# Optimization experiments

Measured on AMD Instinct MI355X. Metric: run time of the kernel, lower is better.

## Reference

```python
import jax, jax.numpy as jnp
import numpy as np

B, L, D_OUT, D_HIDDEN = 16, 4096, 1024, 512
MAX_PHASE = 6.28
R_MIN, R_MAX = 0.9, 0.999


def setup_inputs() -> dict:
    key = jax.random.key(0)
    ks = jax.random.split(key, 8)
    x = jax.random.normal(ks[0], (B, L, D_OUT), dtype=jnp.float32)
    # theta_init: log(max_phase * u)
    u_th = jax.random.uniform(ks[1], (D_HIDDEN,), dtype=jnp.float32)
    theta_log = jnp.log(MAX_PHASE * u_th)
    # nu_init: log(-0.5 * log(u * (r_max^2 - r_min^2) + r_min^2))
    u_nu = jax.random.uniform(ks[2], (D_HIDDEN,), dtype=jnp.float32)
    nu_log = jnp.log(-0.5 * jnp.log(u_nu * (R_MAX**2 - R_MIN**2) + R_MIN**2))
    # gamma_log_init from (nu_log, theta_log)
    diag_lambda = jnp.exp(-jnp.exp(nu_log) + 1j * jnp.exp(theta_log))
    gamma_log = jnp.log(jnp.sqrt(1.0 - jnp.abs(diag_lambda) ** 2))
    b_norm = jnp.sqrt(2.0 * D_OUT)
    c_norm = jnp.sqrt(float(D_HIDDEN))
    B_re = jax.random.normal(ks[3], (D_HIDDEN, D_OUT), dtype=jnp.float32) / b_norm
    B_im = jax.random.normal(ks[4], (D_HIDDEN, D_OUT), dtype=jnp.float32) / b_norm
    C_re = jax.random.normal(ks[5], (D_OUT, D_HIDDEN), dtype=jnp.float32) / c_norm
    C_im = jax.random.normal(ks[6], (D_OUT, D_HIDDEN), dtype=jnp.float32) / c_norm
    D = jax.random.normal(ks[7], (D_OUT,), dtype=jnp.float32)
    return {"x": x, "theta_log": theta_log, "nu_log": nu_log, "gamma_log": gamma_log,
            "B_re": B_re, "B_im": B_im, "C_re": C_re, "C_im": C_im, "D": D}


def _binop(q_i, q_j):
    # associative op for linear recurrence h_t = A_t * h_{t-1} + b_t (diagonal A)
    A_i, b_i = q_i
    A_j, b_j = q_j
    return (A_j * A_i, A_j * b_i + b_j)


def reference(x, theta_log, nu_log, gamma_log, B_re, B_im, C_re, C_im, D):
    diag_lambda = jnp.exp(-jnp.exp(nu_log) + 1j * jnp.exp(theta_log))  # (H,)
    B_norm = (B_re + 1j * B_im) * jnp.exp(gamma_log)[:, None]          # (H, D)
    C = C_re + 1j * C_im                                               # (D, H)
    # input projection: Bu_t = B_norm @ x_t -> (B, L, H) complex
    Bu = jnp.einsum('hd,bld->blh', B_norm, x.astype(B_norm.dtype))
    Lam = jnp.broadcast_to(diag_lambda, Bu.shape)
    # parallel scan over the sequence axis
    _, h = jax.lax.associative_scan(_binop, (Lam, Bu), axis=1)         # (B, L, H)
    # readout: y_t = Re[C h_t] + D * x_t
    y = jnp.einsum('oh,blh->blo', C, h).real + D * x
    return (y, h[:, -1])
```

## Files before the change

kernel.cpp:

```cpp
#include <hip/hip_runtime.h>

#define NB 16
#define NL 4096
#define NDO 1024
#define NH 512
#define NM (NB*NL)
#define NK 1024
#define NN 1024
#define CH 128
#define NCHUNK (NL/CH)
#define YCOUNT ((size_t)NM*NDO)
#define HCOUNT ((size_t)NB*NH)

typedef unsigned short u16;
typedef float f32x4 __attribute__((ext_vector_type(4)));
typedef unsigned int u32x4 __attribute__((ext_vector_type(4)));
typedef __bf16 bf16x8 __attribute__((ext_vector_type(8)));

__device__ __forceinline__ u16 f2bf(float f){
  unsigned u = __float_as_uint(f);
  unsigned r = u + 0x7fffu + ((u >> 16) & 1u);
  return (u16)(r >> 16);
}
__device__ __forceinline__ float bf2f(u16 v){ return __uint_as_float(((unsigned)v) << 16); }
__device__ __forceinline__ unsigned pack2(float a, float b){
  return (unsigned)f2bf(a) | ((unsigned)f2bf(b) << 16);
}

__device__ __forceinline__ void gld_lds16(const u16* g, u16* l){
  __builtin_amdgcn_global_load_lds(
      (const __attribute__((address_space(1))) unsigned int*)g,
      (__attribute__((address_space(3))) unsigned int*)l,
      16, 0, 0);
}


__global__ void prep_w1(const float* __restrict__ Bre, const float* __restrict__ Bim,
                        const float* __restrict__ gl, u16* __restrict__ W1){
  int i = blockIdx.x * blockDim.x + threadIdx.x;
  if (i >= NH * NDO) return;
  int h = i / NDO, d = i % NDO;
  float g = expf(gl[h]);
  W1[(size_t)h * NK + d]        = f2bf(Bre[i] * g);
  W1[(size_t)(NH + h) * NK + d] = f2bf(Bim[i] * g);
}

__global__ void prep_w2(const float* __restrict__ Cre, const float* __restrict__ Cim,
                        u16* __restrict__ W2){
  int i = blockIdx.x * blockDim.x + threadIdx.x;
  if (i >= NDO * NH) return;
  int o = i / NH, k = i % NH;
  W2[(size_t)o * NK + k]      = f2bf(Cre[i]);
  W2[(size_t)o * NK + NH + k] = f2bf(-Cim[i]);
}

__global__ void prep_lam(const float* __restrict__ theta_log, const float* __restrict__ nu_log,
                         float* __restrict__ lam){
  int h = threadIdx.x;
  if (h >= NH) return;
  float nu = expf(nu_log[h]);
  float th = expf(theta_log[h]);
  float mag = expf(-nu);
  float lre = mag * cosf(th), lim = mag * sinf(th);
  double pre = (double)lre, pim = (double)lim;
  #pragma unroll
  for (int s = 0; s < 7; s++){
    double nr = pre*pre - pim*pim;
    double ni = 2.0*pre*pim;
    pre = nr; pim = ni;
  }
  lam[h]        = lre;
  lam[NH + h]   = lim;
  lam[2*NH + h] = (float)pre;
  lam[3*NH + h] = (float)pim;
}

__global__ __launch_bounds__(256) void convert_x(const float* __restrict__ X, u16* __restrict__ Xb){
  size_t i = ((size_t)blockIdx.x * 256 + threadIdx.x) * 8;
  f32x4 a = *(const f32x4*)(X + i);
  f32x4 b = *(const f32x4*)(X + i + 4);
  u32x4 p;
  p[0] = pack2(a[0], a[1]); p[1] = pack2(a[2], a[3]);
  p[2] = pack2(b[0], b[1]); p[3] = pack2(b[2], b[3]);
  *(u32x4*)(Xb + i) = p;
}


#define STG_PAIR(AT, BT, t) do {                                 \
    _Pragma("unroll")                                            \
    for (int s = 0; s < 4; s++){                                 \
      gld_lds16(Ag + (size_t)(t)*64 + (size_t)s*8*NK, &AT[w*32 + s*8][0]); \
      gld_lds16(Bg + (size_t)(t)*64 + (size_t)s*8*NK, &BT[w*32 + s*8][0]); \
    }                                                            \
  } while(0)
#define CMP_TILE(AT, BT) do {                                       \
    bf16x8 af[4][2], bv[4][2];                                      \
    _Pragma("unroll")                                               \
    for (int i = 0; i < 4; i++){                                    \
      const u16* pa = &AT[rowa + i*16][0];                          \
      const u16* pb = &BT[rowb + i*16][0];                          \
      af[i][0] = *(const bf16x8*)(pa + sw0);                        \
      af[i][1] = *(const bf16x8*)(pa + sw1);                        \
      bv[i][0] = *(const bf16x8*)(pb + sw0);                        \
      bv[i][1] = *(const bf16x8*)(pb + sw1);                        \
    }                                                               \
    if constexpr (PRIO) __builtin_amdgcn_s_setprio(1);              \
    _Pragma("unroll")                                               \
    for (int i = 0; i < 4; i++)                                     \
      _Pragma("unroll")                                             \
      for (int j = 0; j < 4; j++){                                  \
        acc[i][j] = __builtin_amdgcn_mfma_f32_16x16x32_bf16(af[i][0], bv[j][0], acc[i][j], 0, 0, 0); \
        acc[i][j] = __builtin_amdgcn_mfma_f32_16x16x32_bf16(af[i][1], bv[j][1], acc[i][j], 0, 0, 0); \
      }                                                             \
    if constexpr (PRIO) __builtin_amdgcn_s_setprio(0);              \
  } while(0)
#define WVM(n)  asm volatile("s_waitcnt vmcnt(" #n ")" ::: "memory")
#define LGKM0() asm volatile("s_waitcnt lgkmcnt(0)" ::: "memory")
#define BARR()  asm volatile("s_barrier" ::: "memory")

template<int MODE, bool PRIO>
__global__ __launch_bounds__(256) void gemm_sz(const u16* __restrict__ A,
                                               const u16* __restrict__ W,
                                               const float* __restrict__ Xf,
                                               const u16* __restrict__ Xh,
                                               const float* __restrict__ Dv,
                                               u16* __restrict__ outB,
                                               float* __restrict__ outF){
  __shared__ __align__(16) u16 A0[128][64];
  __shared__ __align__(16) u16 B0[128][64];
  __shared__ __align__(16) u16 A1[128][64];
  __shared__ __align__(16) u16 B1[128][64];
  const int tid = threadIdx.x;
  const int bid = blockIdx.x;
  const int lid = (bid & 7) * 512 + (bid >> 3);
  const int m0 = (lid >> 3) << 7;
  const int n0 = (lid & 7) << 7;
  const int w = tid >> 6, lane = tid & 63;
  const int wm = w >> 1, wn = w & 1;

  const int grow = lane >> 3;
  const int gcol = ((lane & 7) ^ grow) << 3;
  const u16* Ag = A + (size_t)(m0 + w*32 + grow) * NK + gcol;
  const u16* Bg = W + (size_t)(n0 + w*32 + grow) * NK + gcol;

  f32x4 acc[4][4];
#pragma unroll
  for (int i = 0; i < 4; i++)
#pragma unroll
    for (int j = 0; j < 4; j++) acc[i][j] = (f32x4){0.f,0.f,0.f,0.f};

  const int c15 = lane & 15;
  const int q   = lane >> 4;
  const int sw0 = ((q    ) ^ (lane & 7)) << 3;
  const int sw1 = ((q | 4) ^ (lane & 7)) << 3;
  const int rowa = wm*64 + c15;
  const int rowb = wn*64 + c15;

  STG_PAIR(A0, B0, 0);
  STG_PAIR(A1, B1, 1);
  WVM(8);
  BARR();

  for (int t = 0; t < 14; t += 2) {
    CMP_TILE(A0, B0);
    LGKM0();
    BARR();
    STG_PAIR(A0, B0, t + 2);
    WVM(8);
    BARR();
    CMP_TILE(A1, B1);
    LGKM0();
    BARR();
    STG_PAIR(A1, B1, t + 3);
    WVM(8);
    BARR();
  }
  CMP_TILE(A0, B0);
  WVM(0);
  BARR();
  CMP_TILE(A1, B1);

  const int r0 = (lane >> 4) << 2;
#pragma unroll
  for (int i = 0; i < 4; i++){
    int gm = m0 + wm*64 + i*16 + r0;
#pragma unroll
    for (int j = 0; j < 4; j++){
      int gn = n0 + wn*64 + j*16 + c15;
      if constexpr (MODE == 0) {
#pragma unroll
        for (int r = 0; r < 4; r++)
          outB[(size_t)(gm + r) * NN + gn] = f2bf(acc[i][j][r]);
      } else if constexpr (MODE == 1) {
        float dv = Dv[gn];
#pragma unroll
        for (int r = 0; r < 4; r++){
          size_t oidx = (size_t)(gm + r) * NDO + gn;
          outF[oidx] = acc[i][j][r] + dv * Xf[oidx];
        }
      } else {
        float dv = Dv[gn];
#pragma unroll
        for (int r = 0; r < 4; r++){
          size_t oidx = (size_t)(gm + r) * NDO + gn;
          outF[oidx] = acc[i][j][r] + dv * bf2f(Xh[oidx]);
        }
      }
    }
  }
}


__global__ __launch_bounds__(256) void gemm1_legacy(const float* __restrict__ X,
                                                    const u16* __restrict__ W1,
                                                    u16* __restrict__ Bu){
  __shared__ __align__(16) u16 Alds[128][32];
  __shared__ __align__(16) u16 Blds[128][32];
  const int tid = threadIdx.x;
  const int bid = blockIdx.x;
  const int lid = (bid & 7) * 512 + (bid >> 3);
  const int m0 = (lid >> 3) << 7;
  const int n0 = (lid & 7) << 7;
  const int w = tid >> 6, lane = tid & 63;
  const int wm = w >> 1, wn = w & 1;
  f32x4 acc[4][4];
#pragma unroll
  for (int i = 0; i < 4; i++)
#pragma unroll
    for (int j = 0; j < 4; j++) acc[i][j] = (f32x4){0.f,0.f,0.f,0.f};

  const int srow = tid >> 1;
  const int skseg = (tid & 1) << 4;
  const float* xp = X + (size_t)(m0 + srow) * NK + skseg;
  const u16*  wp  = W1 + (size_t)(n0 + srow) * NK + skseg;

  const int klane = (lane >> 4) << 3;
  const int rowa = wm*64 + (lane & 15);
  const int rowb = wn*64 + (lane & 15);

  for (int k0 = 0; k0 < NK; k0 += 32) {
    __syncthreads();
    f32x4 v0 = *(const f32x4*)(xp + k0 + 0);
    f32x4 v1 = *(const f32x4*)(xp + k0 + 4);
    f32x4 v2 = *(const f32x4*)(xp + k0 + 8);
    f32x4 v3 = *(const f32x4*)(xp + k0 + 12);
    u32x4 q0 = *(const u32x4*)(wp + k0);
    u32x4 q1 = *(const u32x4*)(wp + k0 + 8);
    u32x4 p0, p1;
    p0[0] = pack2(v0[0], v0[1]); p0[1] = pack2(v0[2], v0[3]);
    p0[2] = pack2(v1[0], v1[1]); p0[3] = pack2(v1[2], v1[3]);
    p1[0] = pack2(v2[0], v2[1]); p1[1] = pack2(v2[2], v2[3]);
    p1[2] = pack2(v3[0], v3[1]); p1[3] = pack2(v3[2], v3[3]);
    *(u32x4*)&Alds[srow][skseg]     = p0;
    *(u32x4*)&Alds[srow][skseg + 8] = p1;
    *(u32x4*)&Blds[srow][skseg]     = q0;
    *(u32x4*)&Blds[srow][skseg + 8] = q1;
    __syncthreads();
    bf16x8 af[4], bv[4];
#pragma unroll
    for (int i = 0; i < 4; i++){
      af[i] = *(const bf16x8*)&Alds[rowa + i*16][klane];
      bv[i] = *(const bf16x8*)&Blds[rowb + i*16][klane];
    }
#pragma unroll
    for (int i = 0; i < 4; i++)
#pragma unroll
      for (int j = 0; j < 4; j++)
        acc[i][j] = __builtin_amdgcn_mfma_f32_16x16x32_bf16(af[i], bv[j], acc[i][j], 0, 0, 0);
  }

  const int r0 = (lane >> 4) << 2;
  const int col = lane & 15;
#pragma unroll
  for (int i = 0; i < 4; i++){
    int gm = m0 + wm*64 + i*16 + r0;
#pragma unroll
    for (int j = 0; j < 4; j++){
      int gn = n0 + wn*64 + j*16 + col;
#pragma unroll
      for (int r = 0; r < 4; r++)
        Bu[(size_t)(gm + r) * NN + gn] = f2bf(acc[i][j][r]);
    }
  }
}


__global__ __launch_bounds__(512) void scan_carry(const u16* __restrict__ Bu,
                                                  const float* __restrict__ lam,
                                                  float* __restrict__ carry){
  const int h = threadIdx.x;
  const int bc = blockIdx.x;
  const int b = bc / NCHUNK, c = bc % NCHUNK;
  const float lre = lam[h], lim = lam[NH + h];
  float hre = 0.f, him = 0.f;
  size_t base = (size_t)(b * NL + c * CH) * NN;
  for (int j = 0; j < CH; j++){
    float bre = bf2f(Bu[base + (size_t)j*NN + h]);
    float bim = bf2f(Bu[base + (size_t)j*NN + NH + h]);
    float nre = lre*hre - lim*him + bre;
    float nim = lre*him + lim*hre + bim;
    hre = nre; him = nim;
  }
  size_t ci = ((size_t)bc * NH + h) * 2;
  carry[ci] = hre; carry[ci + 1] = him;
}

__global__ __launch_bounds__(512) void scan_combine(const float* __restrict__ carry,
                                                    const float* __restrict__ lam,
                                                    float* __restrict__ hstart){
  const int h = threadIdx.x;
  const int b = blockIdx.x;
  const float Pre = lam[2*NH + h], Pim = lam[3*NH + h];
  float are = 0.f, aim = 0.f;
  for (int c = 0; c < NCHUNK; c++){
    size_t idx = ((size_t)(b * NCHUNK + c) * NH + h) * 2;
    hstart[idx] = are; hstart[idx + 1] = aim;
    float cre = carry[idx], cim = carry[idx + 1];
    float nre = Pre*are - Pim*aim + cre;
    float nim = Pre*aim + Pim*are + cim;
    are = nre; aim = nim;
  }
}

__global__ __launch_bounds__(512) void scan_fixup_full(u16* __restrict__ Bu,
                                                       const float* __restrict__ lam,
                                                       const float* __restrict__ hstart,
                                                       float* __restrict__ out, int out_size){
  const int h = threadIdx.x;
  const int bc = blockIdx.x;
  const int b = bc / NCHUNK, c = bc % NCHUNK;
  const float lre = lam[h], lim = lam[NH + h];
  size_t si = ((size_t)bc * NH + h) * 2;
  const float sre = hstart[si], sim = hstart[si + 1];
  float hre = 0.f, him = 0.f;
  float pre = lre, pim = lim;
  size_t base = (size_t)(b * NL + c * CH) * NN;
  for (int j = 0; j < CH; j++){
    float bre = bf2f(Bu[base + (size_t)j*NN + h]);
    float bim = bf2f(Bu[base + (size_t)j*NN + NH + h]);
    float nre = lre*hre - lim*him + bre;
    float nim = lre*him + lim*hre + bim;
    hre = nre; him = nim;
    float vre = hre + pre*sre - pim*sim;
    float vim = him + pre*sim + pim*sre;
    Bu[base + (size_t)j*NN + h]      = f2bf(vre);
    Bu[base + (size_t)j*NN + NH + h] = f2bf(vim);
    if (c == NCHUNK - 1 && j == CH - 1){
      size_t ore_i = YCOUNT + (size_t)b * NH + h;
      size_t oim_i = YCOUNT + HCOUNT + (size_t)b * NH + h;
      if (ore_i < (size_t)out_size) out[ore_i] = vre;
      if (oim_i < (size_t)out_size) out[oim_i] = vim;
    }
    float qre = pre*lre - pim*lim;
    float qim = pre*lim + pim*lre;
    pre = qre; pim = qim;
  }
}


extern "C" void kernel_launch(void* const* d_in, const int* in_sizes, int n_in,
                              void* d_out, int out_size, void* d_ws, size_t ws_size,
                              hipStream_t stream) {
  const float* x         = (const float*)d_in[0];
  const float* theta_log = (const float*)d_in[1];
  const float* nu_log    = (const float*)d_in[2];
  const float* gamma_log = (const float*)d_in[3];
  const float* Bre       = (const float*)d_in[4];
  const float* Bim       = (const float*)d_in[5];
  const float* Cre       = (const float*)d_in[6];
  const float* Cim       = (const float*)d_in[7];
  const float* Dv        = (const float*)d_in[8];
  float* out = (float*)d_out;
  char* ws = (char*)d_ws;

  u16*   W1     = (u16*)(ws);
  u16*   W2     = (u16*)(ws + (2u << 20));
  float* lam    = (float*)(ws + (4u << 20));
  float* carry  = (float*)(ws + (5u << 20));
  float* hstart = (float*)(ws + (7u << 20));
  u16*   Bu     = (u16*)(ws + (16u << 20));
  u16*   Xb     = (u16*)(ws + (144u << 20));
  size_t need_base = (16u << 20) + (size_t)NM * NN * 2;
  size_t need_fast = need_base + (size_t)NM * NK * 2;
  if (ws_size < need_base) return;
  const bool fast = (ws_size >= need_fast);

  prep_w1<<<(NH * NDO + 255) / 256, 256, 0, stream>>>(Bre, Bim, gamma_log, W1);
  prep_w2<<<(NDO * NH + 255) / 256, 256, 0, stream>>>(Cre, Cim, W2);
  prep_lam<<<1, 512, 0, stream>>>(theta_log, nu_log, lam);

  if (fast) {
    convert_x<<<(int)(YCOUNT / (256*8)), 256, 0, stream>>>(x, Xb);
    gemm_sz<0, true><<<4096, 256, 0, stream>>>(Xb, W1, nullptr, nullptr, nullptr, Bu, nullptr);
  } else {
    gemm1_legacy<<<4096, 256, 0, stream>>>(x, W1, Bu);
  }

  scan_carry<<<NB * NCHUNK, 512, 0, stream>>>(Bu, lam, carry);
  scan_combine<<<NB, 512, 0, stream>>>(carry, lam, hstart);
  scan_fixup_full<<<NB * NCHUNK, 512, 0, stream>>>(Bu, lam, hstart, out, out_size);

  if (fast) {
    gemm_sz<2, false><<<4096, 256, 0, stream>>>(Bu, W2, nullptr, Xb, Dv, nullptr, out);
  } else {
    gemm_sz<1, false><<<4096, 256, 0, stream>>>(Bu, W2, x, nullptr, Dv, nullptr, out);
  }
}
```

Measured before the change: 561.3 us.

## Use 256x256 tile GEMM with 512 threads for the input projection

Adds a new GEMM kernel with 256x256 output tiles, 8 waves per block, and a double-buffered LDS pipeline. It replaces the 128x128 kernel for the first projection (X·W1) to raise arithmetic intensity and cut global/L2 traffic per flop. It also drops the s_setprio priority hints from the existing kernel. The larger tile needs 128 accumulator floats per lane and 128KB of LDS at one block per CU. That lowers occupancy and puts stricter vmcnt(0)+barrier syncs in the loop, so load latency may be exposed.

Measured after the change: 852.7 us. 1.52x slower.

```diff
diff --git a/kernel.cpp b/kernel.cpp
--- a/kernel.cpp
+++ b/kernel.cpp
@@ -83,6 +83,135 @@
   p[0] = pack2(a[0], a[1]); p[1] = pack2(a[2], a[3]);
   p[2] = pack2(b[0], b[1]); p[3] = pack2(b[2], b[3]);
   *(u32x4*)(Xb + i) = p;
+}
+
+
+__device__ __forceinline__ void stage_tile(const u16* Ag, const u16* Bg, int kt,
+                                           u16 (&AB)[256][64], u16 (&BB)[256][64], int w){
+  const u16* a = Ag + (size_t)kt * 64;
+  const u16* b = Bg + (size_t)kt * 64;
+  #pragma unroll
+  for (int s = 0; s < 4; s++){
+    gld_lds16(a + (size_t)s * 8 * NK, &AB[w*32 + s*8][0]);
+    gld_lds16(b + (size_t)s * 8 * NK, &BB[w*32 + s*8][0]);
+  }
+}
+
+__device__ __forceinline__ void compute_tile(const u16 (&AB)[256][64], const u16 (&BB)[256][64],
+                                             f32x4 (&acc)[8][4], int wr, int wc,
+                                             int c15, int sw0, int sw1){
+  #pragma unroll
+  for (int ks = 0; ks < 2; ks++){
+    const int sw = (ks == 0) ? sw0 : sw1;
+    bf16x8 af[8], bv[4];
+    #pragma unroll
+    for (int i = 0; i < 8; i++)
+      af[i] = *(const bf16x8*)(&AB[wr*128 + i*16 + c15][0] + sw);
+    #pragma unroll
+    for (int j = 0; j < 4; j++)
+      bv[j] = *(const bf16x8*)(&BB[wc*64 + j*16 + c15][0] + sw);
+    #pragma unroll
+    for (int i = 0; i < 8; i++)
+      #pragma unroll
+      for (int j = 0; j < 4; j++)
+        acc[i][j] = __builtin_amdgcn_mfma_f32_16x16x32_bf16(af[i], bv[j], acc[i][j], 0, 0, 0);
+  }
+}
+
+template<int MODE>
+__global__ __launch_bounds__(512, 1) void gemm_256(const u16* __restrict__ A,
+                                                   const u16* __restrict__ W,
+                                                   const float* __restrict__ Xf,
+                                                   const u16* __restrict__ Xh,
+                                                   const float* __restrict__ Dv,
+                                                   u16* __restrict__ outB,
+                                                   float* __restrict__ outF){
+  __shared__ __align__(16) u16 A0[256][64];
+  __shared__ __align__(16) u16 B0[256][64];
+  __shared__ __align__(16) u16 A1[256][64];
+  __shared__ __align__(16) u16 B1[256][64];
+  const int tid = threadIdx.x;
+  const int bid = blockIdx.x;
+  const int lid = (bid & 7) * 128 + (bid >> 3);
+  const int m0 = (lid >> 2) << 8;
+  const int n0 = (lid & 3) << 8;
+  const int w = tid >> 6, lane = tid & 63;
+  const int wr = w >> 2, wc = w & 3;
+
+  const int grow = lane >> 3;
+  const int gcol = ((lane & 7) ^ grow) << 3;
+  const u16* Ag = A + (size_t)(m0 + w*32 + grow) * NK + gcol;
+  const u16* Bg = W + (size_t)(n0 + w*32 + grow) * NK + gcol;
+
+  const int c15 = lane & 15;
+  const int qb  = lane >> 4;
+  const int sw0 = ((qb    ) ^ (lane & 7)) << 3;
+  const int sw1 = ((qb | 4) ^ (lane & 7)) << 3;
+
+  f32x4 acc[8][4];
+  #pragma unroll
+  for (int m = 0; m < 8; m++)
+    #pragma unroll
+    for (int n = 0; n < 4; n++) acc[m][n] = (f32x4){0.f,0.f,0.f,0.f};
+
+#define LGKM0_() asm volatile("s_waitcnt lgkmcnt(0)" ::: "memory")
+#define VM0_()   asm volatile("s_waitcnt vmcnt(0)" ::: "memory")
+#define BAR_()   __builtin_amdgcn_s_barrier()
+
+  stage_tile(Ag, Bg, 0, A0, B0, w);
+  VM0_();
+  BAR_();
+
+  #pragma unroll 1
+  for (int kt = 0; kt < NK/64; kt += 2){
+    stage_tile(Ag, Bg, kt + 1, A1, B1, w);
+    compute_tile(A0, B0, acc, wr, wc, c15, sw0, sw1);
+    LGKM0_();
+    BAR_();
+    VM0_();
+    BAR_();
+    if (kt + 2 < NK/64){
+      stage_tile(Ag, Bg, kt + 2, A0, B0, w);
+      compute_tile(A1, B1, acc, wr, wc, c15, sw0, sw1);
+      LGKM0_(); BAR_();
+      VM0_();  BAR_();
+    } else {
+      compute_tile(A1, B1, acc, wr, wc, c15, sw0, sw1);
+    }
+  }
+
+#undef LGKM0_
+#undef VM0_
+#undef BAR_
+
+  const int r4 = (lane >> 4) << 2;
+  #pragma unroll
+  for (int m = 0; m < 8; m++){
+    int gm = m0 + wr*128 + m*16 + r4;
+    #pragma unroll
+    for (int n = 0; n < 4; n++){
+      int gn = n0 + wc*64 + n*16 + c15;
+      if constexpr (MODE == 0) {
+        #pragma unroll
+        for (int r = 0; r < 4; r++)
+          outB[(size_t)(gm + r) * NN + gn] = f2bf(acc[m][n][r]);
+      } else if constexpr (MODE == 1) {
+        float dv = Dv[gn];
+        #pragma unroll
+        for (int r = 0; r < 4; r++){
+          size_t oidx = (size_t)(gm + r) * NDO + gn;
+          outF[oidx] = acc[m][n][r] + dv * Xf[oidx];
+        }
+      } else {
+        float dv = Dv[gn];
+        #pragma unroll
+        for (int r = 0; r < 4; r++){
+          size_t oidx = (size_t)(gm + r) * NDO + gn;
+          outF[oidx] = acc[m][n][r] + dv * bf2f(Xh[oidx]);
+        }
+      }
+    }
+  }
 }
 
 
@@ -104,7 +233,6 @@
       bv[i][0] = *(const bf16x8*)(pb + sw0);                        \
       bv[i][1] = *(const bf16x8*)(pb + sw1);                        \
     }                                                               \
-    if constexpr (PRIO) __builtin_amdgcn_s_setprio(1);              \
     _Pragma("unroll")                                               \
     for (int i = 0; i < 4; i++)                                     \
       _Pragma("unroll")                                             \
@@ -112,13 +240,12 @@
         acc[i][j] = __builtin_amdgcn_mfma_f32_16x16x32_bf16(af[i][0], bv[j][0], acc[i][j], 0, 0, 0); \
         acc[i][j] = __builtin_amdgcn_mfma_f32_16x16x32_bf16(af[i][1], bv[j][1], acc[i][j], 0, 0, 0); \
       }                                                             \
-    if constexpr (PRIO) __builtin_amdgcn_s_setprio(0);              \
   } while(0)
 #define WVM(n)  asm volatile("s_waitcnt vmcnt(" #n ")" ::: "memory")
 #define LGKM0() asm volatile("s_waitcnt lgkmcnt(0)" ::: "memory")
 #define BARR()  asm volatile("s_barrier" ::: "memory")
 
-template<int MODE, bool PRIO>
+template<int MODE>
 __global__ __launch_bounds__(256) void gemm_sz(const u16* __restrict__ A,
                                                const u16* __restrict__ W,
                                                const float* __restrict__ Xf,
@@ -160,7 +287,6 @@
   STG_PAIR(A1, B1, 1);
   WVM(8);
   BARR();
-
   for (int t = 0; t < 14; t += 2) {
     CMP_TILE(A0, B0);
     LGKM0();
@@ -389,9 +515,11 @@
   prep_w2<<<(NDO * NH + 255) / 256, 256, 0, stream>>>(Cre, Cim, W2);
   prep_lam<<<1, 512, 0, stream>>>(theta_log, nu_log, lam);
 
+  const int g256 = (NM / 256) * (NN / 256);
+
   if (fast) {
     convert_x<<<(int)(YCOUNT / (256*8)), 256, 0, stream>>>(x, Xb);
-    gemm_sz<0, true><<<4096, 256, 0, stream>>>(Xb, W1, nullptr, nullptr, nullptr, Bu, nullptr);
+    gemm_256<0><<<g256, 512, 0, stream>>>(Xb, W1, nullptr, nullptr, nullptr, Bu, nullptr);
   } else {
     gemm1_legacy<<<4096, 256, 0, stream>>>(x, W1, Bu);
   }
@@ -401,8 +529,8 @@
   scan_fixup_full<<<NB * NCHUNK, 512, 0, stream>>>(Bu, lam, hstart, out, out_size);
 
   if (fast) {
-    gemm_sz<2, false><<<4096, 256, 0, stream>>>(Bu, W2, nullptr, Xb, Dv, nullptr, out);
+    gemm_sz<2><<<4096, 256, 0, stream>>>(Bu, W2, nullptr, Xb, Dv, nullptr, out);
   } else {
-    gemm_sz<1, false><<<4096, 256, 0, stream>>>(Bu, W2, x, nullptr, Dv, nullptr, out);
-  }
-}
+    gemm_sz<1><<<4096, 256, 0, stream>>>(Bu, W2, x, nullptr, Dv, nullptr, out);
+  }
+}
```
